# Kernel optimization log

Hardware: AMD Instinct MI355X
Metric: run time of the kernel (lower is better)

The kernel has to match this reference:

```python
import jax, jax.numpy as jnp
import numpy as np

FILTER_LENGTH = 1024
HOP_LENGTH = 512
CUTOFF = FILTER_LENGTH // 2 + 1  # 513


def _make_basis():
    # Real/imag rows of the DFT matrix, matching np.fft.fft(np.eye(N))[:cutoff]
    fb = np.fft.fft(np.eye(FILTER_LENGTH))
    basis = np.vstack([fb[:CUTOFF].real, fb[:CUTOFF].imag]).astype(np.float32)  # [1026, 1024]
    return jnp.asarray(basis)


def setup_inputs() -> dict:
    key = jax.random.key(0)
    input_data = jax.random.normal(key, (16, 2097152), dtype=jnp.float32)
    return {"input_data": input_data, "forward_basis": _make_basis()}


def reference(input_data, forward_basis):
    B, T = input_data.shape
    n_frames = (T - FILTER_LENGTH) // HOP_LENGTH + 1  # valid conv, stride=hop
    # Frame extraction equivalent to conv1d with stride=hop, padding=0
    idx = jnp.arange(n_frames)[:, None] * HOP_LENGTH + jnp.arange(FILTER_LENGTH)[None, :]
    frames = input_data[:, idx]  # [B, n_frames, filter_length]
    # conv1d against DFT basis == frame @ basis^T
    ft = jnp.einsum('bnf,cf->bcn', frames, forward_basis)  # [B, 1026, n_frames]
    real = ft[:, :CUTOFF]
    imag = ft[:, CUTOFF:]
    return jnp.sqrt(real * real + imag * imag)  # [B, 513, n_frames]
```

## Files before the change

kernel.cpp:

```cpp
#include <hip/hip_runtime.h>
#include <math.h>

#define CUTOFF   513
#define NFRAMES  4095
#define TLEN     2097152
#define NBATCH   16
#define NW       4

#define WAVE_SYNC() asm volatile("s_waitcnt lgkmcnt(0)" ::: "memory")

typedef float cplx __attribute__((ext_vector_type(2)));

__device__ __forceinline__ cplx cadd(cplx a, cplx b){
    cplx r; asm("v_pk_add_f32 %0, %1, %2" : "=v"(r) : "v"(a), "v"(b)); return r;
}
__device__ __forceinline__ cplx csub(cplx a, cplx b){
    cplx r; asm("v_pk_add_f32 %0, %1, %2 op_sel:[0,0] op_sel_hi:[1,1] neg_lo:[0,1] neg_hi:[0,1]"
                : "=v"(r) : "v"(a), "v"(b)); return r;
}
__device__ __forceinline__ cplx submul_i(cplx a, cplx b){
    cplx r; asm("v_pk_add_f32 %0, %1, %2 op_sel:[0,1] op_sel_hi:[1,0] neg_hi:[0,1]"
                : "=v"(r) : "v"(a), "v"(b)); return r;
}
__device__ __forceinline__ cplx addmul_i(cplx a, cplx b){
    cplx r; asm("v_pk_add_f32 %0, %1, %2 op_sel:[0,1] op_sel_hi:[1,0] neg_lo:[0,1]"
                : "=v"(r) : "v"(a), "v"(b)); return r;
}
__device__ __forceinline__ cplx cmul(cplx a, cplx b){
    cplx t, r;
    asm("v_pk_mul_f32 %0, %1, %2 op_sel:[1,1] op_sel_hi:[1,0]"
        : "=v"(t) : "v"(a), "v"(b));
    asm("v_pk_fma_f32 %0, %1, %2, %3 op_sel:[0,0,0] op_sel_hi:[0,1,1] neg_lo:[0,0,1]"
        : "=v"(r) : "v"(a), "v"(b), "v"(t));
    return r;
}
__device__ __forceinline__ cplx cmul_mi(cplx a){ return (cplx){a.y, -a.x}; }

__device__ __forceinline__ float fsqrt(float x){
    float r; asm("v_sqrt_f32 %0, %1" : "=v"(r) : "v"(x)); return r;
}

__device__ __forceinline__ void fft16(cplx* A) {
    const float C1 = 0.92387953251f, S1 = 0.38268343236f, HF = 0.70710678119f;
    cplx C[16];
    #pragma unroll
    for (int j4 = 0; j4 < 4; ++j4) {
        cplx a = A[j4], b = A[j4+4], c = A[j4+8], d = A[j4+12];
        cplx t0 = cadd(a,c), t1 = csub(a,c), t2 = cadd(b,d), t3 = csub(b,d);
        C[4*j4+0] = cadd(t0,t2);
        C[4*j4+1] = submul_i(t1,t3);
        C[4*j4+2] = csub(t0,t2);
        C[4*j4+3] = addmul_i(t1,t3);
    }
    C[4*1+1] = cmul(C[4*1+1], (cplx){ C1,-S1});
    C[4*1+2] = cmul(C[4*1+2], (cplx){ HF,-HF});
    C[4*1+3] = cmul(C[4*1+3], (cplx){ S1,-C1});
    C[4*2+1] = cmul(C[4*2+1], (cplx){ HF,-HF});
    C[4*2+2] = cmul_mi(C[4*2+2]);
    C[4*2+3] = cmul(C[4*2+3], (cplx){-HF,-HF});
    C[4*3+1] = cmul(C[4*3+1], (cplx){ S1,-C1});
    C[4*3+2] = cmul(C[4*3+2], (cplx){-HF,-HF});
    C[4*3+3] = cmul(C[4*3+3], (cplx){-C1, S1});
    #pragma unroll
    for (int klo = 0; klo < 4; ++klo) {
        cplx a = C[klo], b = C[4+klo], c = C[8+klo], d = C[12+klo];
        cplx t0 = cadd(a,c), t1 = csub(a,c), t2 = cadd(b,d), t3 = csub(b,d);
        A[klo]    = cadd(t0,t2);
        A[klo+4]  = submul_i(t1,t3);
        A[klo+8]  = csub(t0,t2);
        A[klo+12] = addmul_i(t1,t3);
    }
}

__device__ __forceinline__ void twiddle15(cplx* A, cplx w1) {
    cplx t2  = cmul(w1, w1);
    cplx t3  = cmul(t2, w1);
    cplx t4  = cmul(t2, t2);
    cplx t8  = cmul(t4, t4);
    cplx t12 = cmul(t8, t4);
    A[4]  = cmul(A[4],  t4);  A[5]  = cmul(A[5],  t4);
    A[6]  = cmul(A[6],  t4);  A[7]  = cmul(A[7],  t4);
    A[8]  = cmul(A[8],  t8);  A[9]  = cmul(A[9],  t8);
    A[10] = cmul(A[10], t8);  A[11] = cmul(A[11], t8);
    A[12] = cmul(A[12], t12); A[13] = cmul(A[13], t12);
    A[14] = cmul(A[14], t12); A[15] = cmul(A[15], t12);
    A[1]  = cmul(A[1],  w1);  A[5]  = cmul(A[5],  w1);
    A[9]  = cmul(A[9],  w1);  A[13] = cmul(A[13], w1);
    A[2]  = cmul(A[2],  t2);  A[6]  = cmul(A[6],  t2);
    A[10] = cmul(A[10], t2);  A[14] = cmul(A[14], t2);
    A[3]  = cmul(A[3],  t3);  A[7]  = cmul(A[7],  t3);
    A[11] = cmul(A[11], t3);  A[15] = cmul(A[15], t3);
}

__device__ __forceinline__ void dft4(const cplx* h, cplx* X) {
    cplx t0 = cadd(h[0],h[2]), t1 = csub(h[0],h[2]);
    cplx t2 = cadd(h[1],h[3]), t3 = csub(h[1],h[3]);
    X[0] = cadd(t0,t2);
    X[1] = submul_i(t1,t3);
    X[2] = csub(t0,t2);
    X[3] = addmul_i(t1,t3);
}

__device__ __forceinline__ float2 magpair(cplx Zk, cplx Zm) {
    cplx xs, ys, s;
    asm("v_pk_add_f32 %0, %1, %2 op_sel:[0,0] op_sel_hi:[0,0] neg_hi:[0,1]"
        : "=v"(xs) : "v"(Zk), "v"(Zm));
    asm("v_pk_add_f32 %0, %1, %2 op_sel:[1,1] op_sel_hi:[1,1] neg_lo:[0,1]"
        : "=v"(ys) : "v"(Zk), "v"(Zm));
    asm("v_pk_mul_f32 %0, %1, %1" : "=v"(s) : "v"(xs));
    asm("v_pk_fma_f32 %0, %1, %1, %2" : "=v"(s) : "v"(ys), "v"(s));
    return make_float2(0.5f*fsqrt(s.x), 0.5f*fsqrt(s.y));
}

__global__ __launch_bounds__(256, 5)
void stft_mag_kernel(const float* __restrict__ in, float* __restrict__ out) {
    __shared__ __align__(16) cplx fftb[NW][1024];
    float* mt = (float*)fftb;
    const int tid = threadIdx.x, lane = tid & 63, w = tid >> 6;
    const int H = blockIdx.x;
    const int LB = ((H & 7) << 10) | (H >> 3);
    const int b = LB >> 9, blk = LB & 511;
    const int p = 4 * blk + w;
    const bool noB = (2 * p + 1) >= NFRAMES;
    const float* bi = in + (size_t)b * TLEN;
    float* bo = out + (size_t)b * ((size_t)CUTOFF * NFRAMES);
    cplx* buf = fftb[w];

    float v[24];
    const float* src = bi + 1024 * p + lane;
    #pragma unroll
    for (int t = 0; t < 16; ++t) v[t] = src[64 * t];
    #pragma unroll
    for (int t = 16; t < 24; ++t) v[t] = noB ? 0.f : src[64 * t];
    cplx A[16];
    #pragma unroll
    for (int r = 0; r < 16; ++r) A[r] = (cplx){v[r], noB ? 0.f : v[r + 8]};

    fft16(A);
    {
        float s, c;
        __sincosf((float)lane * 6.135923151542565e-03f, &s, &c);
        twiddle15(A, (cplx){c, -s});
    }
    #pragma unroll
    for (int k = 0; k < 16; ++k)
        buf[64 * k + ((lane + 4 * k) & 63)] = A[k];
    WAVE_SYNC();

    const int k1 = lane & 15, j2 = lane >> 4;
    #pragma unroll
    for (int r = 0; r < 16; ++r)
        A[r] = buf[64 * k1 + ((4 * r + j2 + 4 * k1) & 63)];
    fft16(A);
    {
        float s, c;
        __sincosf((float)j2 * 9.817477042468103e-02f, &s, &c);
        twiddle15(A, (cplx){c, -s});
    }
    WAVE_SYNC();
    #pragma unroll
    for (int k = 0; k < 16; ++k) {
        int sv = k1 ^ k;
        int eo = (sv >> 2) & 1;
        buf[64 * k + 4 * sv + 2 * ((j2 >> 1) ^ eo) + (j2 & 1)] = A[k];
    }
    WAVE_SYNC();

    const int f0 = 2 * w;
    const float4* q4 = (const float4*)buf;
    float ch[16];
    #pragma unroll
    for (int vv = 0; vv < 2; ++vv) {
        const int u = 2 * lane + vv;
        if (u == 0) {
            float4 a0 = q4[0], a1 = q4[1];
            float4 b0 = q4[272], b1 = q4[273];
            cplx hq[4], hp[4];
            hq[0]=(cplx){a0.x,a0.y}; hq[1]=(cplx){a0.z,a0.w}; hq[2]=(cplx){a1.x,a1.y}; hq[3]=(cplx){a1.z,a1.w};
            hp[0]=(cplx){b0.x,b0.y}; hp[1]=(cplx){b0.z,b0.w}; hp[2]=(cplx){b1.x,b1.y}; hp[3]=(cplx){b1.z,b1.w};
            cplx X0[4], X1[4];
            dft4(hq, X0); dft4(hp, X1);
            ch[0] = fabsf(X0[0].x); ch[1] = fabsf(X0[0].y);
            float2 m = magpair(X0[1], X0[3]); ch[2] = m.x; ch[3] = m.y;
            m = magpair(X1[0], X1[3]); ch[4] = m.x; ch[5] = m.y;
            m = magpair(X1[1], X1[2]); ch[6] = m.x; ch[7] = m.y;
            bo[(size_t)512 * NFRAMES + 2 * p] = fabsf(X0[2].x);
            if (!noB) bo[(size_t)512 * NFRAMES + 2 * p + 1] = fabsf(X0[2].y);
        } else {
            const int q = u, qp = 256 - u;
            const int sq = q ^ (q >> 4), sp = qp ^ (qp >> 4);
            const int eq = (sq >> 2) & 1,  ep = (sp >> 2) & 1;
            float4 a0 = q4[2*sq + eq], a1 = q4[2*sq + 1 - eq];
            float4 b0 = q4[2*sp + ep], b1 = q4[2*sp + 1 - ep];
            cplx hq[4], hp[4];
            hq[0]=(cplx){a0.x,a0.y}; hq[1]=(cplx){a0.z,a0.w}; hq[2]=(cplx){a1.x,a1.y}; hq[3]=(cplx){a1.z,a1.w};
            hp[0]=(cplx){b0.x,b0.y}; hp[1]=(cplx){b0.z,b0.w}; hp[2]=(cplx){b1.x,b1.y}; hp[3]=(cplx){b1.z,b1.w};
            cplx Xq[4], Xp[4];
            dft4(hq, Xq); dft4(hp, Xp);
            float2 m;
            m = magpair(Xq[0], Xp[3]); ch[8*vv+0] = m.x; ch[8*vv+1] = m.y;
            m = magpair(Xq[1], Xp[2]); ch[8*vv+2] = m.x; ch[8*vv+3] = m.y;
            m = magpair(Xp[0], Xq[3]); ch[8*vv+4] = m.x; ch[8*vv+5] = m.y;
            m = magpair(Xp[1], Xq[2]); ch[8*vv+6] = m.x; ch[8*vv+7] = m.y;
        }
    }
    __syncthreads();

    auto MTW = [&](int k, int f, float val) {
        mt[8 * k + ((f + (k >> 3)) & 7)] = val;
    };
    #pragma unroll
    for (int vv = 0; vv < 2; ++vv) {
        const int u = 2 * lane + vv;
        if (u == 0) {
            MTW(0,   f0, ch[0]); MTW(0,   f0 + 1, ch[1]);
            MTW(256, f0, ch[2]); MTW(256, f0 + 1, ch[3]);
            MTW(128, f0, ch[4]); MTW(128, f0 + 1, ch[5]);
            MTW(384, f0, ch[6]); MTW(384, f0 + 1, ch[7]);
        } else {
            MTW(u,       f0, ch[8*vv+0]); MTW(u,       f0+1, ch[8*vv+1]);
            MTW(u + 256, f0, ch[8*vv+2]); MTW(u + 256, f0+1, ch[8*vv+3]);
            MTW(256 - u, f0, ch[8*vv+4]); MTW(256 - u, f0+1, ch[8*vv+5]);
            MTW(512 - u, f0, ch[8*vv+6]); MTW(512 - u, f0+1, ch[8*vv+7]);
        }
    }
    __syncthreads();

    #pragma unroll
    for (int i = 0; i < 16; ++i) {
        int L = 256 * i + tid;
        int c = L >> 3, f = L & 7;
        int n = 8 * blk + f;
        if (n < NFRAMES)
            bo[(size_t)c * NFRAMES + n] = mt[8 * c + ((f + (c >> 3)) & 7)];
    }
}

extern "C" void kernel_launch(void* const* d_in, const int* in_sizes, int n_in,
                              void* d_out, int out_size, void* d_ws, size_t ws_size,
                              hipStream_t stream) {
    const float* in = (const float*)d_in[0];
    float* out = (float*)d_out;
    dim3 grid(512 * NBATCH, 1, 1);
    stft_mag_kernel<<<grid, 256, 0, stream>>>(in, out);
}
```

Measured before the change: 244.8 us.

## Load precomputed twiddle table and route bin 512 through padded LDS transpose

Replaces the in-kernel sincos and power-chain twiddle generation with a precomputed twiddle table. The table is built once on the host and copied to workspace on every launch, and each lane reads its twiddles from global memory. The Nyquist bin (512) now goes through the shared-memory transpose, using a row stride of 9 instead of an XOR swizzle, rather than being written directly with scattered stores. The lane-to-u mapping also changes to contiguous. This trades ALU work for extra global loads, a per-call host-to-device copy, and possible LDS bank conflicts from the new stride.

```diff
diff --git a/kernel.cpp b/kernel.cpp
--- a/kernel.cpp
+++ b/kernel.cpp
@@ -6,6 +6,7 @@
 #define TLEN     2097152
 #define NBATCH   16
 #define NW       4
+#define MTS      9
 
 #define WAVE_SYNC() asm volatile("s_waitcnt lgkmcnt(0)" ::: "memory")
 
@@ -72,26 +73,6 @@
     }
 }
 
-__device__ __forceinline__ void twiddle15(cplx* A, cplx w1) {
-    cplx t2  = cmul(w1, w1);
-    cplx t3  = cmul(t2, w1);
-    cplx t4  = cmul(t2, t2);
-    cplx t8  = cmul(t4, t4);
-    cplx t12 = cmul(t8, t4);
-    A[4]  = cmul(A[4],  t4);  A[5]  = cmul(A[5],  t4);
-    A[6]  = cmul(A[6],  t4);  A[7]  = cmul(A[7],  t4);
-    A[8]  = cmul(A[8],  t8);  A[9]  = cmul(A[9],  t8);
-    A[10] = cmul(A[10], t8);  A[11] = cmul(A[11], t8);
-    A[12] = cmul(A[12], t12); A[13] = cmul(A[13], t12);
-    A[14] = cmul(A[14], t12); A[15] = cmul(A[15], t12);
-    A[1]  = cmul(A[1],  w1);  A[5]  = cmul(A[5],  w1);
-    A[9]  = cmul(A[9],  w1);  A[13] = cmul(A[13], w1);
-    A[2]  = cmul(A[2],  t2);  A[6]  = cmul(A[6],  t2);
-    A[10] = cmul(A[10], t2);  A[14] = cmul(A[14], t2);
-    A[3]  = cmul(A[3],  t3);  A[7]  = cmul(A[7],  t3);
-    A[11] = cmul(A[11], t3);  A[15] = cmul(A[15], t3);
-}
-
 __device__ __forceinline__ void dft4(const cplx* h, cplx* X) {
     cplx t0 = cadd(h[0],h[2]), t1 = csub(h[0],h[2]);
     cplx t2 = cadd(h[1],h[3]), t3 = csub(h[1],h[3]);
@@ -113,7 +94,8 @@
 }
 
 __global__ __launch_bounds__(256, 5)
-void stft_mag_kernel(const float* __restrict__ in, float* __restrict__ out) {
+void stft_mag_kernel(const float* __restrict__ in, float* __restrict__ out,
+                     const cplx* __restrict__ twg) {
     __shared__ __align__(16) cplx fftb[NW][1024];
     float* mt = (float*)fftb;
     const int tid = threadIdx.x, lane = tid & 63, w = tid >> 6;
@@ -132,19 +114,22 @@
     for (int t = 0; t < 16; ++t) v[t] = src[64 * t];
     #pragma unroll
     for (int t = 16; t < 24; ++t) v[t] = noB ? 0.f : src[64 * t];
+    cplx tw1[15];
+    #pragma unroll
+    for (int k = 0; k < 15; ++k) tw1[k] = twg[64 * k + lane];
     cplx A[16];
     #pragma unroll
     for (int r = 0; r < 16; ++r) A[r] = (cplx){v[r], noB ? 0.f : v[r + 8]};
 
     fft16(A);
-    {
-        float s, c;
-        __sincosf((float)lane * 6.135923151542565e-03f, &s, &c);
-        twiddle15(A, (cplx){c, -s});
-    }
+    #pragma unroll
+    for (int k = 1; k < 16; ++k) A[k] = cmul(A[k], tw1[k - 1]);
     #pragma unroll
     for (int k = 0; k < 16; ++k)
         buf[64 * k + ((lane + 4 * k) & 63)] = A[k];
+    cplx tw2[15];
+    #pragma unroll
+    for (int k = 0; k < 15; ++k) tw2[k] = twg[960 + 64 * k + lane];
     WAVE_SYNC();
 
     const int k1 = lane & 15, j2 = lane >> 4;
@@ -152,11 +137,8 @@
     for (int r = 0; r < 16; ++r)
         A[r] = buf[64 * k1 + ((4 * r + j2 + 4 * k1) & 63)];
     fft16(A);
-    {
-        float s, c;
-        __sincosf((float)j2 * 9.817477042468103e-02f, &s, &c);
-        twiddle15(A, (cplx){c, -s});
-    }
+    #pragma unroll
+    for (int k = 1; k < 16; ++k) A[k] = cmul(A[k], tw2[k - 1]);
     WAVE_SYNC();
     #pragma unroll
     for (int k = 0; k < 16; ++k) {
@@ -168,10 +150,10 @@
 
     const int f0 = 2 * w;
     const float4* q4 = (const float4*)buf;
-    float ch[16];
+    float ch[16], m512a = 0.f, m512b = 0.f;
     #pragma unroll
     for (int vv = 0; vv < 2; ++vv) {
-        const int u = 2 * lane + vv;
+        const int u = lane + 64 * vv;
         if (u == 0) {
             float4 a0 = q4[0], a1 = q4[1];
             float4 b0 = q4[272], b1 = q4[273];
@@ -184,8 +166,7 @@
             float2 m = magpair(X0[1], X0[3]); ch[2] = m.x; ch[3] = m.y;
             m = magpair(X1[0], X1[3]); ch[4] = m.x; ch[5] = m.y;
             m = magpair(X1[1], X1[2]); ch[6] = m.x; ch[7] = m.y;
-            bo[(size_t)512 * NFRAMES + 2 * p] = fabsf(X0[2].x);
-            if (!noB) bo[(size_t)512 * NFRAMES + 2 * p + 1] = fabsf(X0[2].y);
+            m512a = fabsf(X0[2].x); m512b = fabsf(X0[2].y);
         } else {
             const int q = u, qp = 256 - u;
             const int sq = q ^ (q >> 4), sp = qp ^ (qp >> 4);
@@ -206,17 +187,16 @@
     }
     __syncthreads();
 
-    auto MTW = [&](int k, int f, float val) {
-        mt[8 * k + ((f + (k >> 3)) & 7)] = val;
-    };
+    auto MTW = [&](int k, int f, float val) { mt[MTS * k + f] = val; };
     #pragma unroll
     for (int vv = 0; vv < 2; ++vv) {
-        const int u = 2 * lane + vv;
+        const int u = lane + 64 * vv;
         if (u == 0) {
             MTW(0,   f0, ch[0]); MTW(0,   f0 + 1, ch[1]);
             MTW(256, f0, ch[2]); MTW(256, f0 + 1, ch[3]);
             MTW(128, f0, ch[4]); MTW(128, f0 + 1, ch[5]);
             MTW(384, f0, ch[6]); MTW(384, f0 + 1, ch[7]);
+            MTW(512, f0, m512a); MTW(512, f0 + 1, m512b);
         } else {
             MTW(u,       f0, ch[8*vv+0]); MTW(u,       f0+1, ch[8*vv+1]);
             MTW(u + 256, f0, ch[8*vv+2]); MTW(u + 256, f0+1, ch[8*vv+3]);
@@ -227,12 +207,14 @@
     __syncthreads();
 
     #pragma unroll
-    for (int i = 0; i < 16; ++i) {
+    for (int i = 0; i < 17; ++i) {
         int L = 256 * i + tid;
-        int c = L >> 3, f = L & 7;
-        int n = 8 * blk + f;
-        if (n < NFRAMES)
-            bo[(size_t)c * NFRAMES + n] = mt[8 * c + ((f + (c >> 3)) & 7)];
+        if (L < 513 * 8) {
+            int c = L >> 3, f = L & 7;
+            int n = 8 * blk + f;
+            if (n < NFRAMES)
+                bo[(size_t)c * NFRAMES + n] = mt[MTS * c + f];
+        }
     }
 }
 
@@ -241,6 +223,24 @@
                               hipStream_t stream) {
     const float* in = (const float*)d_in[0];
     float* out = (float*)d_out;
+    static float host_tw[1920 * 2];
+    static bool init = false;
+    if (!init) {
+        for (int k = 1; k < 16; ++k)
+            for (int l = 0; l < 64; ++l) {
+                double a = -2.0 * M_PI * (double)(k * l) / 1024.0;
+                host_tw[2*((k-1)*64 + l) + 0] = (float)cos(a);
+                host_tw[2*((k-1)*64 + l) + 1] = (float)sin(a);
+            }
+        for (int k = 1; k < 16; ++k)
+            for (int l = 0; l < 64; ++l) {
+                double a = -2.0 * M_PI * (double)(k * (l >> 4)) / 64.0;
+                host_tw[2*(960 + (k-1)*64 + l) + 0] = (float)cos(a);
+                host_tw[2*(960 + (k-1)*64 + l) + 1] = (float)sin(a);
+            }
+        init = true;
+    }
+    hipMemcpyAsync(d_ws, host_tw, sizeof(host_tw), hipMemcpyHostToDevice, stream);
     dim3 grid(512 * NBATCH, 1, 1);
-    stft_mag_kernel<<<grid, 256, 0, stream>>>(in, out);
-}
+    stft_mag_kernel<<<grid, 256, 0, stream>>>(in, out, (const cplx*)d_ws);
+}
```

Result: slower. 264.4 us (+8.0%).
